# Kernel tuning notes

Measured on AMD Instinct MI355X. Metric: run time of the kernel, lower is better.

The kernel has to match this reference:

```python
import jax, jax.numpy as jnp
import numpy as np

N_NODES = 100000
N_EDGES = 1600000
IN_F = 128
HEADS1, HID = 8, 8
N_CLASSES = 40


def setup_inputs() -> dict:
    key = jax.random.key(0)
    ks = jax.random.split(key, 12)
    x = jax.random.normal(ks[0], (N_NODES, IN_F), dtype=jnp.float32)
    edge_index = jax.random.randint(ks[1], (2, N_EDGES), 0, N_NODES, dtype=jnp.int32)
    edge_attr = jax.random.uniform(ks[2], (N_EDGES, 1), dtype=jnp.float32)
    s = 0.1
    W1 = jax.random.normal(ks[3], (IN_F, HEADS1 * HID), dtype=jnp.float32) * s
    att_src1 = jax.random.normal(ks[4], (HEADS1, HID), dtype=jnp.float32) * s
    att_dst1 = jax.random.normal(ks[5], (HEADS1, HID), dtype=jnp.float32) * s
    att_edge1 = jax.random.normal(ks[6], (1, HEADS1), dtype=jnp.float32) * s
    W2 = jax.random.normal(ks[7], (HEADS1 * HID, N_CLASSES), dtype=jnp.float32) * s
    att_src2 = jax.random.normal(ks[8], (1, N_CLASSES), dtype=jnp.float32) * s
    att_dst2 = jax.random.normal(ks[9], (1, N_CLASSES), dtype=jnp.float32) * s
    att_edge2 = jax.random.normal(ks[10], (1, 1), dtype=jnp.float32) * s
    return {"x": x, "edge_index": edge_index, "edge_attr": edge_attr,
            "W1": W1, "att_src1": att_src1, "att_dst1": att_dst1, "att_edge1": att_edge1,
            "W2": W2, "att_src2": att_src2, "att_dst2": att_dst2, "att_edge2": att_edge2}


def _egat(x, src, dst, edge_attr, W, a_src, a_dst, a_edge, heads, out_dim, concat):
    """Edge-featured GAT conv: gather -> per-edge attention -> neighborhood softmax -> scatter."""
    n = x.shape[0]
    h = (x @ W).reshape(n, heads, out_dim)                       # [N,H,F]
    h_src = h[src]                                               # [E,H,F]
    logits = (h_src * a_src).sum(-1) + (h[dst] * a_dst).sum(-1)  # [E,H]
    logits = logits + edge_attr @ a_edge                          # edge feature term
    logits = jax.nn.leaky_relu(logits, 0.2)
    m = jax.ops.segment_max(logits, dst, num_segments=n)         # [N,H]
    e = jnp.exp(logits - m[dst])
    denom = jax.ops.segment_sum(e, dst, num_segments=n)
    alpha = e / (denom[dst] + 1e-16)                             # softmax over incoming edges
    out = jax.ops.segment_sum(alpha[:, :, None] * h_src, dst, num_segments=n)  # [N,H,F]
    return out.reshape(n, heads * out_dim) if concat else out.mean(axis=1)


def reference(x, edge_index, edge_attr, W1, att_src1, att_dst1, att_edge1,
              W2, att_src2, att_dst2, att_edge2):
    src, dst = edge_index[0], edge_index[1]
    h = _egat(x, src, dst, edge_attr, W1, att_src1, att_dst1, att_edge1, HEADS1, HID, True)
    h = jax.nn.elu(h)
    out = _egat(h, src, dst, edge_attr, W2, att_src2, att_dst2, att_edge2, 1, N_CLASSES, True)
    return jax.nn.log_softmax(out, axis=1)
```

## Files before the change

kernel.cpp:

```cpp
#include <hip/hip_runtime.h>
#include <math.h>

#define N_NODES 100000
#define N_EDGES 1600000
#define IN_F    128
#define NH1     8
#define HID     8
#define C1      64
#define C2      40

#define EB      4096
#define B1      ((N_EDGES + EB - 1) / EB)
#define NPB     128
#define NBIN    ((N_NODES + NPB - 1) / NPB)
#define S2CAP   2560

#define XCAST_BLKS (N_NODES * IN_F / (256 * 8))
#define WPREP_BLKS 44
#define GEMM1_BLKS ((N_NODES / 16 + 3) / 4)

typedef unsigned short ushort_t;
typedef unsigned int uint_t;
typedef _Float16 half_t;
typedef short short8 __attribute__((ext_vector_type(8)));
typedef float f32x4 __attribute__((ext_vector_type(4)));

__device__ __forceinline__ float lrelu(float x) { return x > 0.f ? x : 0.2f * x; }
__device__ __forceinline__ ushort_t f2bf(float f) {
    uint_t u = __float_as_uint(f);
    u = (u + 0x7FFFu + ((u >> 16) & 1u)) >> 16;
    return (ushort_t)u;
}
__device__ __forceinline__ float bf2f(ushort_t s) {
    return __uint_as_float(((uint_t)s) << 16);
}

__global__ __launch_bounds__(256) void k_prep_hist(
    const float* __restrict__ x, ushort_t* __restrict__ xb,
    const float* __restrict__ W1, ushort_t* __restrict__ W1p,
    const float* __restrict__ W2, ushort_t* __restrict__ W2p,
    const int* __restrict__ ei, int* __restrict__ Hblk)
{
    int b = blockIdx.x;
    if (b < B1) {
        __shared__ int h[NBIN];
        for (int i = threadIdx.x; i < NBIN; i += 256) h[i] = 0;
        __syncthreads();
        int base = b * EB;
        for (int i = threadIdx.x; i < EB; i += 256) {
            int idx = base + i;
            if (idx < N_EDGES) atomicAdd(&h[((uint_t)ei[N_EDGES + idx]) >> 7], 1);
        }
        __syncthreads();
        for (int i = threadIdx.x; i < NBIN; i += 256)
            Hblk[i * B1 + b] = h[i];
        return;
    }
    b -= B1;
    if (b < XCAST_BLKS) {
        size_t i8 = ((size_t)b * 256 + threadIdx.x) * 8;
        float4 a = *(const float4*)(x + i8);
        float4 c = *(const float4*)(x + i8 + 4);
        ushort_t o[8] = {f2bf(a.x), f2bf(a.y), f2bf(a.z), f2bf(a.w),
                         f2bf(c.x), f2bf(c.y), f2bf(c.z), f2bf(c.w)};
        *(int4*)(xb + i8) = *(const int4*)o;
        return;
    }
    int i = (b - XCAST_BLKS) * 256 + threadIdx.x;
    if (i < 8192) {
        int j = i & 7, lane = (i >> 3) & 63, nt = (i >> 9) & 3, s = i >> 11;
        int k = s * 32 + (lane >> 4) * 8 + j;
        int n = nt * 16 + (lane & 15);
        W1p[i] = f2bf(W1[k * C1 + n]);
    } else {
        int i2 = i - 8192;
        if (i2 < 3072) {
            int j = i2 & 7, lane = (i2 >> 3) & 63, khalf = (i2 >> 9) & 1, nt = i2 >> 10;
            int n = nt * 16 + (lane & 15);
            int k = khalf * 32 + (lane >> 4) * 8 + j;
            float v = (n < C2) ? W2[k * C2 + n] : 0.f;
            W2p[i2] = f2bf(v);
        }
    }
}

__global__ __launch_bounds__(512) void k_colscan(
    int* __restrict__ Hblk, int* __restrict__ totB)
{
    __shared__ int s[512];
    int bin = blockIdx.x, t = threadIdx.x;
    int v = (t < B1) ? Hblk[bin * B1 + t] : 0;
    s[t] = v;
    __syncthreads();
    for (int off = 1; off < 512; off <<= 1) {
        int u = (t >= off) ? s[t - off] : 0;
        __syncthreads();
        s[t] += u;
        __syncthreads();
    }
    if (t < B1) Hblk[bin * B1 + t] = s[t] - v;
    if (t == 511) totB[bin] = s[511];
}

__global__ __launch_bounds__(512) void k_basescan(
    const int* __restrict__ totB, int* __restrict__ baseB,
    int* __restrict__ rowptr)
{
    __shared__ int s[512];
    int t = threadIdx.x;
    int run = 0;
    for (int c = 0; c < 2; ++c) {
        int i = c * 512 + t;
        int v = (i < NBIN) ? totB[i] : 0;
        s[t] = v;
        __syncthreads();
        for (int off = 1; off < 512; off <<= 1) {
            int u = (t >= off) ? s[t - off] : 0;
            __syncthreads();
            s[t] += u;
            __syncthreads();
        }
        if (i < NBIN) baseB[i] = s[t] - v + run;
        int tot = s[511];
        __syncthreads();
        run += tot;
    }
    if (t == 0) { baseB[NBIN] = run; rowptr[N_NODES] = run; }
}

__global__ __launch_bounds__(256) void k_gemm1_sc1(
    const ushort_t* __restrict__ xb, const ushort_t* __restrict__ W1p,
    const float* __restrict__ as1, const float* __restrict__ ad1,
    ushort_t* __restrict__ H1, float* __restrict__ s1, float* __restrict__ d1,
    const int* __restrict__ ei, const float* __restrict__ ea,
    const int* __restrict__ Hblk, const int* __restrict__ baseB,
    int2* __restrict__ coarse)
{
    int b = blockIdx.x;
    int t = threadIdx.x;
    if (b < B1) {
        __shared__ int    cnt[NBIN];
        __shared__ int    loff[NBIN];
        __shared__ int    gof[NBIN];
        __shared__ int    ssc[256];
        __shared__ int2   sbuf[EB];
        __shared__ ushort_t sbin[EB];
        int base = b * EB;
        int nE = min(EB, N_EDGES - base);
        for (int i = t; i < NBIN; i += 256) cnt[i] = 0;
        __syncthreads();
        int myb[EB / 256];
        #pragma unroll
        for (int c = 0; c < EB / 256; ++c) {
            int i = base + c * 256 + t;
            int bn = -1;
            if (i < N_EDGES) {
                bn = ((uint_t)ei[N_EDGES + i]) >> 7;
                atomicAdd(&cnt[bn], 1);
            }
            myb[c] = bn;
        }
        __syncthreads();
        {
            int b4 = t * 4;
            int a0 = (b4 + 0 < NBIN) ? cnt[b4 + 0] : 0;
            int a1 = (b4 + 1 < NBIN) ? cnt[b4 + 1] : 0;
            int a2 = (b4 + 2 < NBIN) ? cnt[b4 + 2] : 0;
            int a3 = (b4 + 3 < NBIN) ? cnt[b4 + 3] : 0;
            int tsum = a0 + a1 + a2 + a3;
            ssc[t] = tsum;
            __syncthreads();
            for (int off = 1; off < 256; off <<= 1) {
                int u = (t >= off) ? ssc[t - off] : 0;
                __syncthreads();
                ssc[t] += u;
                __syncthreads();
            }
            int exc = ssc[t] - tsum;
            if (b4 + 0 < NBIN) loff[b4 + 0] = exc;
            if (b4 + 1 < NBIN) loff[b4 + 1] = exc + a0;
            if (b4 + 2 < NBIN) loff[b4 + 2] = exc + a0 + a1;
            if (b4 + 3 < NBIN) loff[b4 + 3] = exc + a0 + a1 + a2;
        }
        __syncthreads();
        for (int i = t; i < NBIN; i += 256) {
            gof[i] = baseB[i] + Hblk[i * B1 + b] - loff[i];
            cnt[i] = loff[i];
        }
        __syncthreads();
        #pragma unroll
        for (int c = 0; c < EB / 256; ++c) {
            int i = base + c * 256 + t;
            if (i < N_EDGES) {
                int bn = myb[c];
                int s = ei[i];
                int d = ei[N_EDGES + i];
                float e = ea[i];
                int p = atomicAdd(&cnt[bn], 1);
                sbuf[p] = make_int2(s | ((d & (NPB - 1)) << 24), __float_as_int(e));
                sbin[p] = (ushort_t)bn;
            }
        }
        __syncthreads();
        for (int j = t; j < nE; j += 256) {
            int bn = sbin[j];
            coarse[gof[bn] + j] = sbuf[j];
        }
        return;
    }
    int tile = ((b - B1) * 256 + t) >> 6;
    int lane = t & 63;
    if (tile >= N_NODES / 16) return;
    int quad = lane >> 4, lo = lane & 15;
    const ushort_t* arow = xb + ((size_t)tile * 16 + lo) * IN_F + quad * 8;
    short8 a0 = *(const short8*)arow;
    short8 a1 = *(const short8*)(arow + 32);
    short8 a2 = *(const short8*)(arow + 64);
    short8 a3 = *(const short8*)(arow + 96);
    f32x4 acc[4] = {{0,0,0,0},{0,0,0,0},{0,0,0,0},{0,0,0,0}};
    #pragma unroll
    for (int nt = 0; nt < 4; ++nt) {
        short8 b0 = *(const short8*)&W1p[((0 * 4 + nt) * 64 + lane) * 8];
        short8 b1 = *(const short8*)&W1p[((1 * 4 + nt) * 64 + lane) * 8];
        short8 b2 = *(const short8*)&W1p[((2 * 4 + nt) * 64 + lane) * 8];
        short8 b3 = *(const short8*)&W1p[((3 * 4 + nt) * 64 + lane) * 8];
        acc[nt] = __builtin_amdgcn_mfma_f32_16x16x32_bf16(a0, b0, acc[nt], 0, 0, 0);
        acc[nt] = __builtin_amdgcn_mfma_f32_16x16x32_bf16(a1, b1, acc[nt], 0, 0, 0);
        acc[nt] = __builtin_amdgcn_mfma_f32_16x16x32_bf16(a2, b2, acc[nt], 0, 0, 0);
        acc[nt] = __builtin_amdgcn_mfma_f32_16x16x32_bf16(a3, b3, acc[nt], 0, 0, 0);
    }
    int nb = tile * 16 + quad * 4;
    float ps[4][4], pd[4][4];
    #pragma unroll
    for (int nt = 0; nt < 4; ++nt) {
        int cb = nt * 16 + lo;
        float av = as1[cb], dv = ad1[cb];
        #pragma unroll
        for (int r = 0; r < 4; ++r) {
            H1[(size_t)(nb + r) * C1 + cb] = f2bf(acc[nt][r]);
            ps[nt][r] = acc[nt][r] * av;
            pd[nt][r] = acc[nt][r] * dv;
        }
    }
    #pragma unroll
    for (int nt = 0; nt < 4; ++nt)
        #pragma unroll
        for (int r = 0; r < 4; ++r)
            #pragma unroll
            for (int off = 1; off < 8; off <<= 1) {
                ps[nt][r] += __shfl_xor(ps[nt][r], off);
                pd[nt][r] += __shfl_xor(pd[nt][r], off);
            }
    if ((lo & 7) == 0) {
        int hh = lo >> 3;
        #pragma unroll
        for (int nt = 0; nt < 4; ++nt) {
            int h = nt * 2 + hh;
            #pragma unroll
            for (int r = 0; r < 4; ++r) {
                s1[(nb + r) * NH1 + h] = ps[nt][r];
                d1[(nb + r) * NH1 + h] = pd[nt][r];
            }
        }
    }
}

__global__ __launch_bounds__(256) void k_scatter2(
    const int2* __restrict__ coarse, const int* __restrict__ baseB,
    int2* __restrict__ edges, int* __restrict__ rowptr)
{
    __shared__ int2 buf[S2CAP];
    __shared__ int h[NPB];
    __shared__ int ofx[NPB];
    __shared__ int ssc[256];
    int bin = blockIdx.x, t = threadIdx.x;
    int s0 = baseB[bin], s1b = baseB[bin + 1];
    int n = s1b - s0;
    if (t < NPB) h[t] = 0;
    __syncthreads();
    for (int j = t; j < n; j += 256)
        atomicAdd(&h[(uint_t)coarse[s0 + j].x >> 24], 1);
    __syncthreads();
    int v = (t < NPB) ? h[t] : 0;
    ssc[t] = v;
    __syncthreads();
    for (int off = 1; off < 256; off <<= 1) {
        int u = (t >= off) ? ssc[t - off] : 0;
        __syncthreads();
        ssc[t] += u;
        __syncthreads();
    }
    int exc = ssc[t] - v;
    if (t < NPB) {
        ofx[t] = exc;
        int node = bin * NPB + t;
        if (node < N_NODES) rowptr[node] = s0 + exc;
        h[t] = exc;
    }
    __syncthreads();
    for (int j = t; j < n; j += 256) {
        int2 c = coarse[s0 + j];
        int ln = (uint_t)c.x >> 24;
        int p = atomicAdd(&h[ln], 1);
        int2 ov = make_int2(c.x & 0x00FFFFFF, c.y);
        if (p < S2CAP) buf[p] = ov;
        else           edges[s0 + p] = ov;
    }
    __syncthreads();
    int nl = n < S2CAP ? n : S2CAP;
    for (int j = t; j < nl; j += 256)
        edges[s0 + j] = buf[j];
}


__global__ __launch_bounds__(256) void k_node1(
    const int* __restrict__ rowptr, const int2* __restrict__ edges,
    const float* __restrict__ s1, const float* __restrict__ d1,
    const float* __restrict__ ae1,
    const ushort_t* __restrict__ H1, ushort_t* __restrict__ out1r)
{
    __shared__ uint_t sm_s[4][64];
    __shared__ float  sm_pf[4][8][65];
    int w = (blockIdx.x * blockDim.x + threadIdx.x) >> 6;
    int lane = threadIdx.x & 63;
    int wv = (threadIdx.x >> 6) & 3;
    if (w >= N_NODES) return;
    int half = lane >> 5, lo32 = lane & 31;
    int h = lo32 >> 2;
    uint_t fb = (uint_t)lo32 << 2;
    int jb = rowptr[w], je = rowptr[w + 1];
    float4 d1a = *(const float4*)(d1 + w * NH1);
    float4 d1b = *(const float4*)(d1 + w * NH1 + 4);
    float4 aea = *(const float4*)(ae1);
    float4 aeb = *(const float4*)(ae1 + 4);
    float den = 0.f, acc0 = 0.f, acc1 = 0.f;
    const float* pfh = sm_pf[wv][h];
    for (int base = jb; base < je; base += 64) {
        int idx = base + lane;
        uint_t soff = 0;
        float pf[8] = {0.f, 0.f, 0.f, 0.f, 0.f, 0.f, 0.f, 0.f};
        if (idx < je) {
            int2 ed = edges[idx];
            soff = (uint_t)ed.x << 7;
            float ea = __int_as_float(ed.y);
            const float* s1r = s1 + (size_t)ed.x * NH1;
            float4 sa = *(const float4*)s1r;
            float4 sb = *(const float4*)(s1r + 4);
            pf[0] = __expf(lrelu(fmaf(ea, aea.x, sa.x + d1a.x)));
            pf[1] = __expf(lrelu(fmaf(ea, aea.y, sa.y + d1a.y)));
            pf[2] = __expf(lrelu(fmaf(ea, aea.z, sa.z + d1a.z)));
            pf[3] = __expf(lrelu(fmaf(ea, aea.w, sa.w + d1a.w)));
            pf[4] = __expf(lrelu(fmaf(ea, aeb.x, sb.x + d1b.x)));
            pf[5] = __expf(lrelu(fmaf(ea, aeb.y, sb.y + d1b.y)));
            pf[6] = __expf(lrelu(fmaf(ea, aeb.z, sb.z + d1b.z)));
            pf[7] = __expf(lrelu(fmaf(ea, aeb.w, sb.w + d1b.w)));
        }
        sm_s[wv][lane] = soff;
        #pragma unroll
        for (int k = 0; k < 8; ++k) sm_pf[wv][k][lane] = pf[k];
        __builtin_amdgcn_wave_barrier();
        int cnt4 = (min(64, je - base) + 3) & ~3;
        for (int e = half; e < cnt4; e += 4) {
            uint_t soA = sm_s[wv][e];
            uint_t soB = sm_s[wv][e + 2];
            float pA = pfh[e];
            float pB = pfh[e + 2];
            uint_t uA = *(const uint_t*)((const char*)H1 + (soA + fb));
            uint_t uB = *(const uint_t*)((const char*)H1 + (soB + fb));
            den += pA + pB;
            acc0 = fmaf(pA, __uint_as_float(uA << 16), acc0);
            acc1 = fmaf(pA, __uint_as_float(uA & 0xffff0000u), acc1);
            acc0 = fmaf(pB, __uint_as_float(uB << 16), acc0);
            acc1 = fmaf(pB, __uint_as_float(uB & 0xffff0000u), acc1);
        }
        __builtin_amdgcn_wave_barrier();
    }
    acc0 += __shfl_xor(acc0, 32);
    acc1 += __shfl_xor(acc1, 32);
    den  += __shfl_xor(den, 32);
    float inv = 1.f / (den + 1e-16f);
    float o0 = acc0 * inv, o1 = acc1 * inv;
    float r0 = o0 > 0.f ? o0 : __expf(o0) - 1.f;
    float r1 = o1 > 0.f ? o1 : __expf(o1) - 1.f;
    if (half == 0) {
        uint_t pk = (uint_t)f2bf(r0) | ((uint_t)f2bf(r1) << 16);
        *(uint_t*)((char*)out1r + (size_t)w * 128 + fb) = pk;
    }
}

__global__ __launch_bounds__(256) void k_gemm2(
    const ushort_t* __restrict__ out1r, const ushort_t* __restrict__ W2p,
    const float* __restrict__ as2, const float* __restrict__ ad2,
    ushort_t* __restrict__ H2, float* __restrict__ s2, float* __restrict__ d2)
{
    int tile = (blockIdx.x * blockDim.x + threadIdx.x) >> 6;
    int lane = threadIdx.x & 63;
    if (tile >= N_NODES / 16) return;
    int quad = lane >> 4, lo = lane & 15;
    const ushort_t* arow = out1r + ((size_t)tile * 16 + lo) * C1 + quad * 8;
    short8 a0 = *(const short8*)arow;
    short8 a1 = *(const short8*)(arow + 32);
    f32x4 acc[3] = {{0,0,0,0},{0,0,0,0},{0,0,0,0}};
    #pragma unroll
    for (int nt = 0; nt < 3; ++nt) {
        short8 b0 = *(const short8*)&W2p[((nt * 2 + 0) * 64 + lane) * 8];
        short8 b1 = *(const short8*)&W2p[((nt * 2 + 1) * 64 + lane) * 8];
        acc[nt] = __builtin_amdgcn_mfma_f32_16x16x32_bf16(a0, b0, acc[nt], 0, 0, 0);
        acc[nt] = __builtin_amdgcn_mfma_f32_16x16x32_bf16(a1, b1, acc[nt], 0, 0, 0);
    }
    float ps0 = 0.f, ps1 = 0.f, ps2 = 0.f, ps3 = 0.f;
    float pd0 = 0.f, pd1 = 0.f, pd2 = 0.f, pd3 = 0.f;
    #pragma unroll
    for (int nt = 0; nt < 3; ++nt) {
        int cb = nt * 16 + lo;
        float a2 = cb < C2 ? as2[cb] : 0.f;
        float b2 = cb < C2 ? ad2[cb] : 0.f;
        float v0 = acc[nt][0], v1 = acc[nt][1], v2 = acc[nt][2], v3 = acc[nt][3];
        int nb = tile * 16 + quad * 4;
        H2[(size_t)(nb + 0) * C1 + cb] = f2bf(v0);
        H2[(size_t)(nb + 1) * C1 + cb] = f2bf(v1);
        H2[(size_t)(nb + 2) * C1 + cb] = f2bf(v2);
        H2[(size_t)(nb + 3) * C1 + cb] = f2bf(v3);
        ps0 = fmaf(v0, a2, ps0); ps1 = fmaf(v1, a2, ps1);
        ps2 = fmaf(v2, a2, ps2); ps3 = fmaf(v3, a2, ps3);
        pd0 = fmaf(v0, b2, pd0); pd1 = fmaf(v1, b2, pd1);
        pd2 = fmaf(v2, b2, pd2); pd3 = fmaf(v3, b2, pd3);
    }
    #pragma unroll
    for (int off = 1; off < 16; off <<= 1) {
        ps0 += __shfl_xor(ps0, off); ps1 += __shfl_xor(ps1, off);
        ps2 += __shfl_xor(ps2, off); ps3 += __shfl_xor(ps3, off);
        pd0 += __shfl_xor(pd0, off); pd1 += __shfl_xor(pd1, off);
        pd2 += __shfl_xor(pd2, off); pd3 += __shfl_xor(pd3, off);
    }
    if (lo == 0) {
        int nb = tile * 16 + quad * 4;
        s2[nb + 0] = ps0; s2[nb + 1] = ps1; s2[nb + 2] = ps2; s2[nb + 3] = ps3;
        d2[nb + 0] = pd0; d2[nb + 1] = pd1; d2[nb + 2] = pd2; d2[nb + 3] = pd3;
    }
}

__global__ __launch_bounds__(256) void k_node2(
    const int* __restrict__ rowptr, const int2* __restrict__ edges,
    const float* __restrict__ s2, const float* __restrict__ d2,
    const float* __restrict__ ae2,
    const ushort_t* __restrict__ H2, float* __restrict__ out)
{
    __shared__ int2 sp[4][64];
    int w = (blockIdx.x * blockDim.x + threadIdx.x) >> 6;
    int lane = threadIdx.x & 63;
    int wv = (threadIdx.x >> 6) & 3;
    if (w >= N_NODES) return;
    int half = lane >> 5, lo32 = lane & 31;
    int fi = lo32 < 20 ? lo32 : 19;
    uint_t fb = (uint_t)fi << 2;
    int jb = rowptr[w], je = rowptr[w + 1];
    float d2v = d2[w];
    float aev = ae2[0];
    float den = 0.f, acc0 = 0.f, acc1 = 0.f;
    for (int base = jb; base < je; base += 64) {
        int idx = base + lane;
        int soff = 0; float p = 0.f;
        if (idx < je) {
            int2 ed = edges[idx];
            soff = ed.x << 7;
            p = __expf(lrelu(s2[ed.x] + d2v + __int_as_float(ed.y) * aev));
        }
        sp[wv][lane] = make_int2(soff, __float_as_int(p));
        __builtin_amdgcn_wave_barrier();
        int cnt4 = (min(64, je - base) + 3) & ~3;
        for (int e = half; e < cnt4; e += 4) {
            int2 edA = sp[wv][e];
            int2 edB = sp[wv][e + 2];
            uint_t uA = *(const uint_t*)((const char*)H2 + ((uint_t)edA.x + fb));
            uint_t uB = *(const uint_t*)((const char*)H2 + ((uint_t)edB.x + fb));
            float pA = __int_as_float(edA.y);
            float pB = __int_as_float(edB.y);
            den += pA + pB;
            acc0 = fmaf(pA, __uint_as_float(uA << 16), acc0);
            acc1 = fmaf(pA, __uint_as_float(uA & 0xffff0000u), acc1);
            acc0 = fmaf(pB, __uint_as_float(uB << 16), acc0);
            acc1 = fmaf(pB, __uint_as_float(uB & 0xffff0000u), acc1);
        }
        __builtin_amdgcn_wave_barrier();
    }
    acc0 += __shfl_xor(acc0, 32);
    acc1 += __shfl_xor(acc1, 32);
    den  += __shfl_xor(den, 32);
    float inv = 1.f / (den + 1e-16f);
    float o0 = acc0 * inv, o1 = acc1 * inv;
    float v0 = lo32 < 20 ? o0 : -INFINITY;
    float v1 = lo32 < 20 ? o1 : -INFINITY;
    float m = fmaxf(v0, v1);
    #pragma unroll
    for (int off = 16; off; off >>= 1) m = fmaxf(m, __shfl_xor(m, off));
    float pp = lo32 < 20 ? __expf(v0 - m) + __expf(v1 - m) : 0.f;
    #pragma unroll
    for (int off = 16; off; off >>= 1) pp += __shfl_xor(pp, off);
    float ls = __logf(pp);
    if (half == 0 && lo32 < 20) {
        float2 st = make_float2(v0 - m - ls, v1 - m - ls);
        *(float2*)(out + (size_t)w * C2 + 2 * fi) = st;
    }
}

extern "C" void kernel_launch(void* const* d_in, const int* in_sizes, int n_in,
                              void* d_out, int out_size, void* d_ws, size_t ws_size,
                              hipStream_t stream)
{
    const float* x   = (const float*)d_in[0];
    const int*   ei  = (const int*)  d_in[1];
    const float* ea  = (const float*)d_in[2];
    const float* W1  = (const float*)d_in[3];
    const float* as1 = (const float*)d_in[4];
    const float* ad1 = (const float*)d_in[5];
    const float* ae1 = (const float*)d_in[6];
    const float* W2  = (const float*)d_in[7];
    const float* as2 = (const float*)d_in[8];
    const float* ad2 = (const float*)d_in[9];
    const float* ae2 = (const float*)d_in[10];
    float* out = (float*)d_out;

    float*    ws     = (float*)d_ws;
    ushort_t* H1     = (ushort_t*)ws;
    ushort_t* H2     = (ushort_t*)ws;
    ushort_t* out1r  = (ushort_t*)(ws + 3200000);
    int*      Hblk   = (int*)(ws + 3200000);
    int*      totB   = (int*)(ws + 3510000);
    int*      baseB  = (int*)(ws + 3511000);
    int2*     coarse = (int2*)(ws + 6400000);
    ushort_t* xb     = (ushort_t*)(ws + 9600000);
    int2*     edges  = (int2*)(ws + 9600000);
    float*    s1     = ws + 16000000;
    float*    d1     = ws + 16800000;
    int*      rowptr = (int*)(ws + 17600000);
    float*    s2     = ws + 17700008;
    float*    d2     = ws + 17800008;
    ushort_t* W2p    = (ushort_t*)(ws + 17900008);
    ushort_t* W1p    = (ushort_t*)(ws + 17901544);

    k_prep_hist <<<B1 + XCAST_BLKS + WPREP_BLKS, 256, 0, stream>>>(
        x, xb, W1, W1p, W2, W2p, ei, Hblk);
    k_colscan   <<<NBIN, 512, 0, stream>>>(Hblk, totB);
    k_basescan  <<<1, 512, 0, stream>>>(totB, baseB, rowptr);
    k_gemm1_sc1 <<<B1 + GEMM1_BLKS, 256, 0, stream>>>(
        xb, W1p, as1, ad1, H1, s1, d1, ei, ea, Hblk, baseB, coarse);
    k_scatter2  <<<NBIN, 256, 0, stream>>>(coarse, baseB, edges, rowptr);
    k_node1     <<<(N_NODES + 3) / 4, 256, 0, stream>>>(rowptr, edges, s1, d1, ae1,
                                                        H1, out1r);
    k_gemm2     <<<(N_NODES / 16 + 3) / 4, 256, 0, stream>>>(out1r, W2p, as2, ad2,
                                                             H2, s2, d2);
    k_node2     <<<(N_NODES + 3) / 4, 256, 0, stream>>>(rowptr, edges, s2, d2, ae2,
                                                        H2, out);
}
```

Measured before the change: 290.8 us.

## Fuse x bf16 conversion into GEMM1 loads and halve edge block size

Removes the separate x-to-bf16 cast pass and its 25.6MB intermediate buffer. GEMM1 now reads fp32 x directly and converts it to bf16 in registers. The edge block size for the histogram and coarse sort drops from 4096 to 2048, doubling the number of edge blocks. The column scan becomes two 512-wide chunks to handle more than 512 blocks, and the workspace offsets for totB and baseB move because Hblk grows. This saves a full read-and-write pass over x, at the cost of GEMM1 reading twice as many bytes and a longer scan.

```diff
diff --git a/kernel.cpp b/kernel.cpp
--- a/kernel.cpp
+++ b/kernel.cpp
@@ -9,13 +9,12 @@
 #define C1      64
 #define C2      40
 
-#define EB      4096
+#define EB      2048
 #define B1      ((N_EDGES + EB - 1) / EB)
 #define NPB     128
 #define NBIN    ((N_NODES + NPB - 1) / NPB)
 #define S2CAP   2560
 
-#define XCAST_BLKS (N_NODES * IN_F / (256 * 8))
 #define WPREP_BLKS 44
 #define GEMM1_BLKS ((N_NODES / 16 + 3) / 4)
 
@@ -34,9 +33,15 @@
 __device__ __forceinline__ float bf2f(ushort_t s) {
     return __uint_as_float(((uint_t)s) << 16);
 }
+__device__ __forceinline__ short8 ld8f2bf(const float* p) {
+    float4 a = *(const float4*)p;
+    float4 b = *(const float4*)(p + 4);
+    ushort_t o[8] = {f2bf(a.x), f2bf(a.y), f2bf(a.z), f2bf(a.w),
+                     f2bf(b.x), f2bf(b.y), f2bf(b.z), f2bf(b.w)};
+    return *(const short8*)o;
+}
 
 __global__ __launch_bounds__(256) void k_prep_hist(
-    const float* __restrict__ x, ushort_t* __restrict__ xb,
     const float* __restrict__ W1, ushort_t* __restrict__ W1p,
     const float* __restrict__ W2, ushort_t* __restrict__ W2p,
     const int* __restrict__ ei, int* __restrict__ Hblk)
@@ -56,17 +61,7 @@
             Hblk[i * B1 + b] = h[i];
         return;
     }
-    b -= B1;
-    if (b < XCAST_BLKS) {
-        size_t i8 = ((size_t)b * 256 + threadIdx.x) * 8;
-        float4 a = *(const float4*)(x + i8);
-        float4 c = *(const float4*)(x + i8 + 4);
-        ushort_t o[8] = {f2bf(a.x), f2bf(a.y), f2bf(a.z), f2bf(a.w),
-                         f2bf(c.x), f2bf(c.y), f2bf(c.z), f2bf(c.w)};
-        *(int4*)(xb + i8) = *(const int4*)o;
-        return;
-    }
-    int i = (b - XCAST_BLKS) * 256 + threadIdx.x;
+    int i = (b - B1) * 256 + threadIdx.x;
     if (i < 8192) {
         int j = i & 7, lane = (i >> 3) & 63, nt = (i >> 9) & 3, s = i >> 11;
         int k = s * 32 + (lane >> 4) * 8 + j;
@@ -89,17 +84,24 @@
 {
     __shared__ int s[512];
     int bin = blockIdx.x, t = threadIdx.x;
-    int v = (t < B1) ? Hblk[bin * B1 + t] : 0;
-    s[t] = v;
-    __syncthreads();
-    for (int off = 1; off < 512; off <<= 1) {
-        int u = (t >= off) ? s[t - off] : 0;
-        __syncthreads();
-        s[t] += u;
-        __syncthreads();
-    }
-    if (t < B1) Hblk[bin * B1 + t] = s[t] - v;
-    if (t == 511) totB[bin] = s[511];
+    int run = 0;
+    for (int c = 0; c < 2; ++c) {
+        int i = c * 512 + t;
+        int v = (i < B1) ? Hblk[bin * B1 + i] : 0;
+        s[t] = v;
+        __syncthreads();
+        for (int off = 1; off < 512; off <<= 1) {
+            int u = (t >= off) ? s[t - off] : 0;
+            __syncthreads();
+            s[t] += u;
+            __syncthreads();
+        }
+        if (i < B1) Hblk[bin * B1 + i] = s[t] - v + run;
+        int tot = s[511];
+        __syncthreads();
+        run += tot;
+    }
+    if (t == 0) totB[bin] = run;
 }
 
 __global__ __launch_bounds__(512) void k_basescan(
@@ -129,7 +131,7 @@
 }
 
 __global__ __launch_bounds__(256) void k_gemm1_sc1(
-    const ushort_t* __restrict__ xb, const ushort_t* __restrict__ W1p,
+    const float* __restrict__ x, const ushort_t* __restrict__ W1p,
     const float* __restrict__ as1, const float* __restrict__ ad1,
     ushort_t* __restrict__ H1, float* __restrict__ s1, float* __restrict__ d1,
     const int* __restrict__ ei, const float* __restrict__ ea,
@@ -212,11 +214,11 @@
     int lane = t & 63;
     if (tile >= N_NODES / 16) return;
     int quad = lane >> 4, lo = lane & 15;
-    const ushort_t* arow = xb + ((size_t)tile * 16 + lo) * IN_F + quad * 8;
-    short8 a0 = *(const short8*)arow;
-    short8 a1 = *(const short8*)(arow + 32);
-    short8 a2 = *(const short8*)(arow + 64);
-    short8 a3 = *(const short8*)(arow + 96);
+    const float* arow = x + ((size_t)tile * 16 + lo) * IN_F + quad * 8;
+    short8 a0 = ld8f2bf(arow);
+    short8 a1 = ld8f2bf(arow + 32);
+    short8 a2 = ld8f2bf(arow + 64);
+    short8 a3 = ld8f2bf(arow + 96);
     f32x4 acc[4] = {{0,0,0,0},{0,0,0,0},{0,0,0,0},{0,0,0,0}};
     #pragma unroll
     for (int nt = 0; nt < 4; ++nt) {
@@ -526,10 +528,9 @@
     ushort_t* H2     = (ushort_t*)ws;
     ushort_t* out1r  = (ushort_t*)(ws + 3200000);
     int*      Hblk   = (int*)(ws + 3200000);
-    int*      totB   = (int*)(ws + 3510000);
-    int*      baseB  = (int*)(ws + 3511000);
+    int*      totB   = (int*)(ws + 3820000);
+    int*      baseB  = (int*)(ws + 3821000);
     int2*     coarse = (int2*)(ws + 6400000);
-    ushort_t* xb     = (ushort_t*)(ws + 9600000);
     int2*     edges  = (int2*)(ws + 9600000);
     float*    s1     = ws + 16000000;
     float*    d1     = ws + 16800000;
@@ -539,12 +540,12 @@
     ushort_t* W2p    = (ushort_t*)(ws + 17900008);
     ushort_t* W1p    = (ushort_t*)(ws + 17901544);
 
-    k_prep_hist <<<B1 + XCAST_BLKS + WPREP_BLKS, 256, 0, stream>>>(
-        x, xb, W1, W1p, W2, W2p, ei, Hblk);
+    k_prep_hist <<<B1 + WPREP_BLKS, 256, 0, stream>>>(
+        W1, W1p, W2, W2p, ei, Hblk);
     k_colscan   <<<NBIN, 512, 0, stream>>>(Hblk, totB);
     k_basescan  <<<1, 512, 0, stream>>>(totB, baseB, rowptr);
     k_gemm1_sc1 <<<B1 + GEMM1_BLKS, 256, 0, stream>>>(
-        xb, W1p, as1, ad1, H1, s1, d1, ei, ea, Hblk, baseB, coarse);
+        x, W1p, as1, ad1, H1, s1, d1, ei, ea, Hblk, baseB, coarse);
     k_scatter2  <<<NBIN, 256, 0, stream>>>(coarse, baseB, edges, rowptr);
     k_node1     <<<(N_NODES + 3) / 4, 256, 0, stream>>>(rowptr, edges, s1, d1, ae1,
                                                         H1, out1r);
```

Result: no change. 286.3 us (-1.6%).
